# Kernel optimization log

Measured on AMD Instinct MI355X. Metric: run time of the kernel, lower is better.

Reference implementation:

```python
import jax, jax.numpy as jnp
import numpy as np

RADIUS = 1.0 / 16.0
MAX_NEIGHBORS = 64  # forward() passes max_num_neighbors=64
N_POINTS = 16384
N_CLOUDS = 8


def _radius_neighbors(pos, batch, r, k):
    """Dense radius graph: for each point, up to k in-radius same-cloud neighbors.
    Returns idx [N,k] int32 and mask [N,k] bool. loop=True -> self always valid."""
    sq = jnp.sum(pos * pos, axis=-1)                        # [N]
    d2 = sq[:, None] + sq[None, :] - 2.0 * (pos @ pos.T)    # [N,N]
    d2 = jnp.maximum(d2, 0.0)
    valid = (d2 <= r * r) & (batch[:, None] == batch[None, :])
    score = jnp.where(valid, -d2, -jnp.inf)
    vals, idx = jax.lax.top_k(score, k)                     # nearest-first, [N,k]
    mask = vals > -jnp.inf
    return idx, mask


def _point_conv(x, pos, idx, mask, W1, b1, W2, b2):
    """PointNetConv: msg = relu(Linear([x_j, pos_j - pos_i])), max-agg, Linear."""
    xj = x[idx]                                   # [N,K,c_in]  gather
    rel = pos[idx] - pos[:, None, :]              # [N,K,3]
    h = jnp.concatenate([xj, rel], axis=-1) @ W1 + b1   # [N,K,c_mid]
    h = jax.nn.relu(h)
    h = jnp.where(mask[..., None], h, -jnp.inf)
    agg = jnp.max(h, axis=1)                      # [N,c_mid]  max aggregation
    agg = jnp.where(jnp.isfinite(agg), agg, 0.0)  # safety (loop=True makes this moot)
    return agg @ W2 + b2                          # [N,c_out]


def setup_inputs() -> dict:
    key = jax.random.key(0)
    ks = jax.random.split(key, 16)
    pos = jax.random.uniform(ks[0], (N_POINTS, 3), dtype=jnp.float32)
    rgb = jax.random.uniform(ks[1], (N_POINTS, 3), dtype=jnp.float32)
    batch = jnp.sort(jax.random.randint(ks[2], (N_POINTS,), 0, N_CLOUDS)).astype(jnp.int64)

    def lin(k, fan_in, fan_out):
        kw, kb = jax.random.split(k)
        bound = 1.0 / np.sqrt(fan_in)
        W = jax.random.uniform(kw, (fan_in, fan_out), jnp.float32, -bound, bound)
        b = jax.random.uniform(kb, (fan_out,), jnp.float32, -bound, bound)
        return W, b

    W1a, b1a = lin(ks[3], 3 + 3, 8)
    W2a, b2a = lin(ks[4], 8, 8)
    W1b, b1b = lin(ks[5], 8 + 3, 16)
    W2b, b2b = lin(ks[6], 16, 16)
    W1c, b1c = lin(ks[7], 16 + 3, 32)
    W2c, b2c = lin(ks[8], 32, 32)
    return {"pos": pos, "rgb": rgb, "batch": batch,
            "W1a": W1a, "b1a": b1a, "W2a": W2a, "b2a": b2a,
            "W1b": W1b, "b1b": b1b, "W2b": W2b, "b2b": b2b,
            "W1c": W1c, "b1c": b1c, "W2c": W2c, "b2c": b2c}


def reference(pos, rgb, batch,
              W1a, b1a, W2a, b2a,
              W1b, b1b, W2b, b2b,
              W1c, b1c, W2c, b2c):
    # NOTE: rgb is accepted by the original forward() but never used.
    idx, mask = _radius_neighbors(pos, batch, RADIUS, MAX_NEIGHBORS)
    out = jax.nn.celu(_point_conv(pos, pos, idx, mask, W1a, b1a, W2a, b2a))
    out = jax.nn.celu(_point_conv(out, pos, idx, mask, W1b, b1b, W2b, b2b))
    out = jax.nn.celu(_point_conv(out, pos, idx, mask, W1c, b1c, W2c, b2c))
    return pos, out, batch
```

## Files before the change

### kernel.cpp

```cpp
#include <hip/hip_runtime.h>
#include <math.h>

#define N_POINTS 16384
#define CELLS_PER_CLOUD 4096
#define N_CELLS 32768
#define CAP 16
#define NBR_STRIDE 32

constexpr double R2D = 1.0 / 256.0;

__device__ int g_cnt[N_CELLS];

__global__ __launch_bounds__(256) void k_prep(const float* __restrict__ pos,
                                              const int* __restrict__ batch,
                                              float* __restrict__ out,
                                              float4* __restrict__ bucket,
                                              float4* __restrict__ pos4)
{
    int i = blockIdx.x * 256 + threadIdx.x;
    out[i]                = pos[i];
    out[i + N_POINTS]     = pos[i + N_POINTS];
    out[i + 2 * N_POINTS] = pos[i + 2 * N_POINTS];
    out[3 * N_POINTS + 32 * N_POINTS + i] = (float)batch[i];

    float x = pos[3 * i], y = pos[3 * i + 1], z = pos[3 * i + 2];
    int ix = min(max((int)(x * 16.f), 0), 15);
    int iy = min(max((int)(y * 16.f), 0), 15);
    int iz = min(max((int)(z * 16.f), 0), 15);
    int cell = ((batch[i] * 16 + iz) * 16 + iy) * 16 + ix;
    pos4[i] = make_float4(x, y, z, __int_as_float(cell));
    int slot = atomicAdd(&g_cnt[cell], 1);
    if (slot < CAP) bucket[cell * CAP + slot] = make_float4(x, y, z, __int_as_float(i));
}

__global__ __launch_bounds__(512) void k_search_a(
    const float4* __restrict__ pos4, const float4* __restrict__ bucket,
    const float* __restrict__ W1, const float* __restrict__ b1,
    const float* __restrict__ W2, const float* __restrict__ b2,
    float* __restrict__ out_a, float4* __restrict__ nbr, int* __restrict__ nbr_cnt)
{
    __shared__ float sW1[48], sB1[8], sW2[64], sB2[8];
    __shared__ float4 s_hits[NBR_STRIDE][32];
    __shared__ int   s_k[32];
    __shared__ float s_mx[32][9];

    int t = threadIdx.x;
    int p = t & 31;
    int g = t >> 5;

    if (t < 48) sW1[t] = W1[t];
    if (t < 8) { sB1[t] = b1[t]; sB2[t] = b2[t]; }
    if (t < 64) sW2[t] = W2[t];
    if (t < 32) s_k[t] = 0;
    __syncthreads();

    int i = blockIdx.x * 32 + p;
    float4 pi4 = pos4[i];
    float xi = pi4.x, yi = pi4.y, zi = pi4.z;
    double xd = (double)xi, yd = (double)yi, zd = (double)zi;
    int cell0 = __float_as_int(pi4.w);
    int ix = cell0 & 15, iy = (cell0 >> 4) & 15, iz = (cell0 >> 8) & 15;
    int cb = cell0 & ~(CELLS_PER_CLOUD - 1);

    int n[2], cid[2];
#pragma unroll
    for (int cc = 0; cc < 2; cc++) {
        int c = g + 16 * cc;
        int dz = c / 9 - 1, dy = (c / 3) % 3 - 1, dx = c % 3 - 1;
        int zz = iz + dz, yy = iy + dy, xx = ix + dx;
        bool ok = (c < 27) & ((zz | yy | xx) >= 0) & (zz < 16) & (yy < 16) & (xx < 16);
        int zc = min(max(zz, 0), 15), yc = min(max(yy, 0), 15),
            xc = min(max(xx, 0), 15);
        cid[cc] = cb + (zc << 8) + (yc << 4) + xc;
        int nc = min(g_cnt[cid[cc]], CAP);
        n[cc] = ok ? nc : 0;
    }
    int nmax = max(n[0], n[1]);

    for (int s = 0; s < nmax; s++) {
#pragma unroll
        for (int cc = 0; cc < 2; cc++) {
            if (s < n[cc]) {
                float4 q = bucket[cid[cc] * CAP + s];
                double ddx = xd - (double)q.x, ddy = yd - (double)q.y,
                       ddz = zd - (double)q.z;
                double d2 = ddx * ddx + ddy * ddy + ddz * ddz;
                if (d2 <= R2D) {
                    int slot = atomicAdd(&s_k[p], 1);
                    if (slot < NBR_STRIDE) {
                        s_hits[slot][p] = q;
                        nbr[i * NBR_STRIDE + slot] = q;
                    }
                }
            }
        }
    }
    __syncthreads();
    int kc = min(s_k[p], NBR_STRIDE);

    if (g == 0) nbr_cnt[i] = kc;

    if (g < 8) {
        float mxv = 0.f;
        for (int kk = 0; kk < kc; kk++) {
            float4 q = s_hits[kk][p];
            float in6[6] = { q.x, q.y, q.z, q.x - xi, q.y - yi, q.z - zi };
            float h = sB1[g];
#pragma unroll
            for (int c6 = 0; c6 < 6; c6++) h = fmaf(in6[c6], sW1[c6 * 8 + g], h);
            mxv = fmaxf(mxv, fmaxf(h, 0.f));
        }
        s_mx[p][g] = mxv;
    }
    __syncthreads();
    if (g < 8) {
        float o = sB2[g];
#pragma unroll
        for (int k = 0; k < 8; k++) o = fmaf(s_mx[p][k], sW2[k * 8 + g], o);
        out_a[i * 8 + g] = o > 0.f ? o : expm1f(o);
    }
}

template<int CIN4, int CMID, int PTS, bool ZERO_CNT>
__global__ __launch_bounds__(256) void k_conv(
    const float4* __restrict__ pos4, const float4* __restrict__ xin4,
    const float4* __restrict__ nbr, const int* __restrict__ nbr_cnt,
    const float* __restrict__ W1, const float* __restrict__ b1,
    const float* __restrict__ W2, const float* __restrict__ b2,
    float* __restrict__ xout)
{
    constexpr int CIN = CIN4 * 4;
    __shared__ float4 s_q[PTS][NBR_STRIDE];
    __shared__ float4 s_x[PTS][NBR_STRIDE][CIN4];
    __shared__ float  s_agg[PTS][CMID + 1];

    int tid = threadIdx.x;

    if (ZERO_CNT) {
        int gid = blockIdx.x * 256 + tid;
        if (gid < N_CELLS) g_cnt[gid] = 0;
    }

#pragma unroll
    for (int w = tid; w < PTS * NBR_STRIDE; w += 256) {
        int sp = w >> 5, slot = w & 31;
        int si = blockIdx.x * PTS + sp;
        if (slot < nbr_cnt[si]) {
            float4 q = nbr[si * NBR_STRIDE + slot];
            s_q[sp][slot] = q;
            int j = __float_as_int(q.w);
#pragma unroll
            for (int k = 0; k < CIN4; k++) s_x[sp][slot][k] = xin4[j * CIN4 + k];
        }
    }
    __syncthreads();

    int p = tid / CMID;
    int m = tid % CMID;
    int i = blockIdx.x * PTS + p;

    float4 pi = pos4[i];
    int cnt = nbr_cnt[i];

    float w1c[CIN + 3];
#pragma unroll
    for (int k = 0; k < CIN + 3; k++) w1c[k] = W1[k * CMID + m];
    float w2c[CMID];
#pragma unroll
    for (int k = 0; k < CMID; k++) w2c[k] = W2[k * CMID + m];
    float bb = b1[m];

    float mxv = 0.f;
    for (int t = 0; t < cnt; t++) {
        float4 q = s_q[p][t];
        float h = bb;
#pragma unroll
        for (int k = 0; k < CIN4; k++) {
            float4 v = s_x[p][t][k];
            h = fmaf(v.x, w1c[4 * k],     h);
            h = fmaf(v.y, w1c[4 * k + 1], h);
            h = fmaf(v.z, w1c[4 * k + 2], h);
            h = fmaf(v.w, w1c[4 * k + 3], h);
        }
        h = fmaf(q.x - pi.x, w1c[CIN],     h);
        h = fmaf(q.y - pi.y, w1c[CIN + 1], h);
        h = fmaf(q.z - pi.z, w1c[CIN + 2], h);
        mxv = fmaxf(mxv, fmaxf(h, 0.f));
    }
    s_agg[p][m] = mxv;
    __syncthreads();

    float o = b2[m];
#pragma unroll
    for (int k = 0; k < CMID; k++) o = fmaf(s_agg[p][k], w2c[k], o);
    xout[i * CMID + m] = o > 0.f ? o : expm1f(o);
}

extern "C" void kernel_launch(void* const* d_in, const int* in_sizes, int n_in,
                              void* d_out, int out_size, void* d_ws, size_t ws_size,
                              hipStream_t stream)
{
    const float* pos   = (const float*)d_in[0];
    const int*   batch = (const int*)d_in[2];
    const float* W1a = (const float*)d_in[3];
    const float* b1a = (const float*)d_in[4];
    const float* W2a = (const float*)d_in[5];
    const float* b2a = (const float*)d_in[6];
    const float* W1b = (const float*)d_in[7];
    const float* b1b = (const float*)d_in[8];
    const float* W2b = (const float*)d_in[9];
    const float* b2b = (const float*)d_in[10];
    const float* W1c = (const float*)d_in[11];
    const float* b1c = (const float*)d_in[12];
    const float* W2c = (const float*)d_in[13];
    const float* b2c = (const float*)d_in[14];

    float* out = (float*)d_out;

    char* ws = (char*)d_ws;
    size_t off = 0;
    auto alloc = [&](size_t bytes) {
        char* p = ws + off; off += (bytes + 255) & ~size_t(255); return p;
    };
    float4* bucket  = (float4*)alloc((size_t)N_CELLS * CAP * 16);
    float4* pos4    = (float4*)alloc(N_POINTS * 16);
    int*    nbr_cnt = (int*)alloc(N_POINTS * 4);
    float4* nbr     = (float4*)alloc((size_t)N_POINTS * NBR_STRIDE * 16);
    float*  out_a   = (float*)alloc(N_POINTS * 8 * 4);
    float*  out_b   = (float*)alloc(N_POINTS * 16 * 4);

    hipLaunchKernelGGL(k_prep, dim3(N_POINTS / 256), dim3(256), 0, stream,
                       pos, batch, out, bucket, pos4);
    hipLaunchKernelGGL(k_search_a, dim3(N_POINTS / 32), dim3(512), 0, stream,
                       pos4, bucket, W1a, b1a, W2a, b2a,
                       out_a, nbr, nbr_cnt);
    hipLaunchKernelGGL((k_conv<2, 16, 16, false>), dim3(N_POINTS / 16), dim3(256), 0, stream,
                       pos4, (const float4*)out_a, nbr, nbr_cnt,
                       W1b, b1b, W2b, b2b, out_b);
    hipLaunchKernelGGL((k_conv<4, 32, 8, true>), dim3(N_POINTS / 8), dim3(256), 0, stream,
                       pos4, (const float4*)out_b, nbr, nbr_cnt,
                       W1c, b1c, W2c, b2c, out + 3 * N_POINTS);
}
```

Before: 110.4 us.

## Remap search threads so each 32-lane group handles one point's 27 cells

The neighbor search kernel now assigns one 32-thread group per query point, with each lane scanning a single neighboring cell (27 of 32 lanes active), instead of 16 groups each scanning two cells across 32 points. The block shrinks to 256 threads covering 8 points, and the grid grows accordingly. The aim is to remove the two-cell inner loop and the divergence from the max-count loop, and to spread the work over more blocks. In exchange, 5 lanes per group sit idle. The shared atomics on s_k also now contend within a wavefront on the same point, and the later MLP phase uses only 8 of 256 threads per point set, which lowers that phase's utilization.

```diff
diff --git a/kernel.cpp b/kernel.cpp
--- a/kernel.cpp
+++ b/kernel.cpp
@@ -33,28 +33,27 @@
     if (slot < CAP) bucket[cell * CAP + slot] = make_float4(x, y, z, __int_as_float(i));
 }
 
-__global__ __launch_bounds__(512) void k_search_a(
+__global__ __launch_bounds__(256) void k_search_a(
     const float4* __restrict__ pos4, const float4* __restrict__ bucket,
     const float* __restrict__ W1, const float* __restrict__ b1,
     const float* __restrict__ W2, const float* __restrict__ b2,
     float* __restrict__ out_a, float4* __restrict__ nbr, int* __restrict__ nbr_cnt)
 {
     __shared__ float sW1[48], sB1[8], sW2[64], sB2[8];
-    __shared__ float4 s_hits[NBR_STRIDE][32];
-    __shared__ int   s_k[32];
-    __shared__ float s_mx[32][9];
+    __shared__ float4 s_hits[NBR_STRIDE][8];
+    __shared__ int   s_k[8];
+    __shared__ float s_mx[8][9];
 
     int t = threadIdx.x;
-    int p = t & 31;
-    int g = t >> 5;
+    int p = t >> 5;
+    int g = t & 31;
 
     if (t < 48) sW1[t] = W1[t];
-    if (t < 8) { sB1[t] = b1[t]; sB2[t] = b2[t]; }
+    if (t < 8) { sB1[t] = b1[t]; sB2[t] = b2[t]; s_k[t] = 0; }
     if (t < 64) sW2[t] = W2[t];
-    if (t < 32) s_k[t] = 0;
-    __syncthreads();
-
-    int i = blockIdx.x * 32 + p;
+    __syncthreads();
+
+    int i = blockIdx.x * 8 + p;
     float4 pi4 = pos4[i];
     float xi = pi4.x, yi = pi4.y, zi = pi4.z;
     double xd = (double)xi, yd = (double)yi, zd = (double)zi;
@@ -62,36 +61,25 @@
     int ix = cell0 & 15, iy = (cell0 >> 4) & 15, iz = (cell0 >> 8) & 15;
     int cb = cell0 & ~(CELLS_PER_CLOUD - 1);
 
-    int n[2], cid[2];
-#pragma unroll
-    for (int cc = 0; cc < 2; cc++) {
-        int c = g + 16 * cc;
-        int dz = c / 9 - 1, dy = (c / 3) % 3 - 1, dx = c % 3 - 1;
-        int zz = iz + dz, yy = iy + dy, xx = ix + dx;
-        bool ok = (c < 27) & ((zz | yy | xx) >= 0) & (zz < 16) & (yy < 16) & (xx < 16);
-        int zc = min(max(zz, 0), 15), yc = min(max(yy, 0), 15),
-            xc = min(max(xx, 0), 15);
-        cid[cc] = cb + (zc << 8) + (yc << 4) + xc;
-        int nc = min(g_cnt[cid[cc]], CAP);
-        n[cc] = ok ? nc : 0;
-    }
-    int nmax = max(n[0], n[1]);
-
-    for (int s = 0; s < nmax; s++) {
-#pragma unroll
-        for (int cc = 0; cc < 2; cc++) {
-            if (s < n[cc]) {
-                float4 q = bucket[cid[cc] * CAP + s];
-                double ddx = xd - (double)q.x, ddy = yd - (double)q.y,
-                       ddz = zd - (double)q.z;
-                double d2 = ddx * ddx + ddy * ddy + ddz * ddz;
-                if (d2 <= R2D) {
-                    int slot = atomicAdd(&s_k[p], 1);
-                    if (slot < NBR_STRIDE) {
-                        s_hits[slot][p] = q;
-                        nbr[i * NBR_STRIDE + slot] = q;
-                    }
-                }
+    int dz = g / 9 - 1, dy = (g / 3) % 3 - 1, dx = g % 3 - 1;
+    int zz = iz + dz, yy = iy + dy, xx = ix + dx;
+    bool ok = (g < 27) & ((zz | yy | xx) >= 0) & (zz < 16) & (yy < 16) & (xx < 16);
+    int zc = min(max(zz, 0), 15), yc = min(max(yy, 0), 15),
+        xc = min(max(xx, 0), 15);
+    int cid = cb + (zc << 8) + (yc << 4) + xc;
+    int nc = min(g_cnt[cid], CAP);
+    int n = ok ? nc : 0;
+
+    for (int s = 0; s < n; s++) {
+        float4 q = bucket[cid * CAP + s];
+        double ddx = xd - (double)q.x, ddy = yd - (double)q.y,
+               ddz = zd - (double)q.z;
+        double d2 = ddx * ddx + ddy * ddy + ddz * ddz;
+        if (d2 <= R2D) {
+            int slot = atomicAdd(&s_k[p], 1);
+            if (slot < NBR_STRIDE) {
+                s_hits[slot][p] = q;
+                nbr[i * NBR_STRIDE + slot] = q;
             }
         }
     }
@@ -231,7 +219,7 @@
 
     hipLaunchKernelGGL(k_prep, dim3(N_POINTS / 256), dim3(256), 0, stream,
                        pos, batch, out, bucket, pos4);
-    hipLaunchKernelGGL(k_search_a, dim3(N_POINTS / 32), dim3(512), 0, stream,
+    hipLaunchKernelGGL(k_search_a, dim3(N_POINTS / 8), dim3(256), 0, stream,
                        pos4, bucket, W1a, b1a, W2a, b2a,
                        out_a, nbr, nbr_cnt);
     hipLaunchKernelGGL((k_conv<2, 16, 16, false>), dim3(N_POINTS / 16), dim3(256), 0, stream,
```

After: 110.5 us. No clear change (+0.2%).
